# Kernel tuning notes

Hardware: AMD Instinct MI355X
Metric: run time of the kernel (lower is better)

The kernel has to match this reference:

```python
import jax, jax.numpy as jnp
import numpy as np
import math

B, L, D, H = 8, 1024, 768, 12
DH = D // H
MAX_NORM = 1.0 - 1e-5
EPS = 1e-15

def _beta_fn(a, b):
    return math.exp(math.lgamma(a) + math.lgamma(b) - math.lgamma(a + b))

# beta-split scaling factor from Hyperbolic Neural Networks++ (Shimizu et al.)
BETA_RATIO = _beta_fn(DH / 2.0, 0.5) / _beta_fn(D / 2.0, 0.5)

def _artanh(x):
    return jnp.arctanh(jnp.clip(x, -MAX_NORM, MAX_NORM))

def _norm(x):
    return jnp.sqrt(jnp.maximum(jnp.sum(x * x, -1, keepdims=True), EPS * EPS))

def _project(x):
    # clip points back inside the Poincare ball (c=1)
    return x * jnp.minimum(1.0, MAX_NORM / _norm(x))

def _expmap0(v):
    n = _norm(v)
    return jnp.tanh(n) * v / n

def _logmap0(x):
    n = _norm(x)
    return _artanh(n) * x / n

def _mobius_add(x, y):
    x2 = jnp.sum(x * x, -1, keepdims=True)
    y2 = jnp.sum(y * y, -1, keepdims=True)
    xy = jnp.sum(x * y, -1, keepdims=True)
    num = (1.0 + 2.0 * xy + y2) * x + (1.0 - x2) * y
    den = 1.0 + 2.0 * xy + x2 * y2
    return num / jnp.maximum(den, EPS)

def _mobius_matvec(W, x):
    xn = _norm(x)
    mx = x @ W.T
    mxn = _norm(mx)
    return _project(jnp.tanh(mxn / xn * _artanh(xn)) * mx / mxn)

def _hyp_linear(x, W, b=None):
    y = _mobius_matvec(W, x)
    if b is not None:
        y = _project(_mobius_add(y, b))
    return y

def _beta_split(x):
    # (..., D) -> (..., H, DH): logmap0, split heads, beta-rescale, expmap0
    v = _logmap0(x)
    v = v.reshape(v.shape[:-1] + (H, DH)) * BETA_RATIO
    return _expmap0(v)

def _beta_concat(x):
    # (..., H, DH) -> (..., D)
    v = _logmap0(x) / BETA_RATIO
    v = v.reshape(v.shape[:-2] + (D,))
    return _expmap0(v)

def _pairwise_dist(q, k):
    # closed form: d(x,y) = 2 artanh(||-x (+) y||),
    # ||-x (+) y||^2 = ||x-y||^2 / (1 - 2<x,y> + ||x||^2 ||y||^2)
    q2 = jnp.sum(q * q, -1)  # (B,H,Lq)
    k2 = jnp.sum(k * k, -1)  # (B,H,Lk)
    qk = jnp.einsum('bhqd,bhkd->bhqk', q, k)
    diff2 = jnp.maximum(q2[..., :, None] + k2[..., None, :] - 2.0 * qk, 0.0)
    den = jnp.maximum(1.0 - 2.0 * qk + q2[..., :, None] * k2[..., None, :], EPS)
    t = jnp.sqrt(jnp.maximum(diff2 / den, 0.0))
    return 2.0 * _artanh(t)

def _mobius_scalar_mul(r, x):
    n = _norm(x)
    return jnp.tanh(r * _artanh(n)) * x / n

def _weighted_midpoint(v, w):
    # v: (B,H,Lk,DH) points on ball, w: (B,H,Lq,Lk) weights (geoopt-style)
    lam = 2.0 / jnp.maximum(1.0 - jnp.sum(v * v, -1), EPS)  # conformal factor (B,H,Lk)
    den = jnp.einsum('bhqk,bhk->bhq', w, lam - 1.0)[..., None]
    den = jnp.where(jnp.abs(den) < 1e-10, 1e-10, den)
    nom = jnp.einsum('bhqk,bhkd->bhqd', w, lam[..., None] * v)
    two_mean = nom / den
    return _project(_mobius_scalar_mul(0.5, two_mean))


def setup_inputs() -> dict:
    key = jax.random.key(0)
    ks = jax.random.split(key, 7)
    # points inside the ball: expmap0 of small tangent vectors (norm ~0.55)
    x = _project(_expmap0(0.02 * jax.random.normal(ks[0], (B, L, D), jnp.float32)))
    Wq = jax.random.normal(ks[1], (D, D), jnp.float32) / math.sqrt(D)
    Wk = jax.random.normal(ks[2], (D, D), jnp.float32) / math.sqrt(D)
    Wv = jax.random.normal(ks[3], (D, D), jnp.float32) / math.sqrt(D)
    Wp = jax.random.normal(ks[4], (D, D), jnp.float32) / math.sqrt(D)
    bp = _project(0.01 * jax.random.normal(ks[5], (D,), jnp.float32))
    scale = jnp.array(1.0, jnp.float32)
    return {"x": x, "Wq": Wq, "Wk": Wk, "Wv": Wv, "Wp": Wp, "bp": bp, "scale": scale}


def reference(x, Wq, Wk, Wv, Wp, bp, scale):
    # q/k/v hyperbolic linear (no bias), beta-split into heads -> (B,H,L,DH)
    q = jnp.swapaxes(_beta_split(_hyp_linear(x, Wq)), 1, 2)
    k = jnp.swapaxes(_beta_split(_hyp_linear(x, Wk)), 1, 2)
    v = jnp.swapaxes(_beta_split(_hyp_linear(x, Wv)), 1, 2)
    attn = jax.nn.softmax(scale * -_pairwise_dist(q, k), axis=-1)  # (B,H,L,L)
    y = _weighted_midpoint(v, attn)                 # (B,H,L,DH)
    y = _beta_concat(jnp.swapaxes(y, 1, 2))         # (B,L,D)
    y = _hyp_linear(y, Wp, bp)
    return y, attn
```

## Files before the change

kernel.cpp:

```cpp
#include <hip/hip_runtime.h>
#include <hip/hip_bf16.h>
#include <math.h>

namespace {

constexpr int Bb = 8, Ll = 1024, Dd = 768, Hh = 12, DHh = 64;
constexpr int DDm = Dd * Dd;
constexpr float MAXN = 1.0f - 1e-5f;
constexpr float EPSf = 1e-15f;

typedef __attribute__((ext_vector_type(8))) short short8;
typedef __attribute__((ext_vector_type(4))) short short4v;
typedef __attribute__((ext_vector_type(4))) float f32x4;

__device__ __forceinline__ float wred64(float v) {
#pragma unroll
  for (int m = 32; m >= 1; m >>= 1) v += __shfl_xor(v, m, 64);
  return v;
}

__device__ __forceinline__ float artanh_(float x) {
  return 0.5f * logf((1.0f + x) / (1.0f - x));
}

__device__ __forceinline__ void bsplit(float x, unsigned short& h,
                                       unsigned short& l) {
  __hip_bfloat16 hb = __float2bfloat16(x);
  const float hf = __bfloat162float(hb);
  __hip_bfloat16 lb = __float2bfloat16(x - hf);
  h = *(unsigned short*)&hb;
  l = *(unsigned short*)&lb;
}

__device__ __forceinline__ unsigned short bhi(float x) {
  __hip_bfloat16 hb = __float2bfloat16(x);
  return *(unsigned short*)&hb;
}

__device__ __forceinline__ float bf2f(unsigned short u) {
  union { unsigned int i; float f; } cv;
  cv.i = ((unsigned int)u) << 16;
  return cv.f;
}

__device__ __forceinline__ void gll16(const unsigned short* g,
                                      unsigned short* l) {
  __builtin_amdgcn_global_load_lds(
      (const __attribute__((address_space(1))) void*)g,
      (__attribute__((address_space(3))) void*)l, 16, 0, 0);
}

__global__ __launch_bounds__(768) void k_cvtx(const float* __restrict__ x,
                                              unsigned short* __restrict__ hi,
                                              float* __restrict__ xn2a) {
  const int t = threadIdx.x;
  const int row = blockIdx.x;
  const int w = t >> 6, lane = t & 63;
  __shared__ float red[12];
  const float xe = x[(size_t)row * Dd + t];
  hi[(size_t)row * Dd + t] = bhi(xe);
  const float s = wred64(xe * xe);
  if (lane == 0) red[w] = s;
  __syncthreads();
  if (t == 0) {
    float tot = 0.0f;
#pragma unroll
    for (int i = 0; i < 12; i++) tot += red[i];
    xn2a[row] = tot;
  }
}

__global__ __launch_bounds__(256) void k_cvt4(
    const float* __restrict__ w0, const float* __restrict__ w1,
    const float* __restrict__ w2, const float* __restrict__ w3,
    unsigned short* __restrict__ hi) {
  const int z = blockIdx.z;
  const float* in = (z == 0) ? w0 : (z == 1) ? w1 : (z == 2) ? w2 : w3;
  const int i = blockIdx.x * 256 + threadIdx.x;
  if (i >= DDm / 4) return;
  float4 v = ((const float4*)in)[i];
  ((ushort4*)(hi + (size_t)z * DDm))[i] =
      make_ushort4(bhi(v.x), bhi(v.y), bhi(v.z), bhi(v.w));
}

__global__ __launch_bounds__(256) void k_gemm_bf16h(
    const unsigned short* __restrict__ Ahi,
    const unsigned short* __restrict__ Whi, float* __restrict__ C) {
  constexpr int K = Dd, N = Dd;
  const int z = blockIdx.z;
  const unsigned short* Bh = Whi + (size_t)z * DDm;
  float* Cz = C + (size_t)z * 8192 * N;
  __shared__ __align__(16) unsigned short sAh[128 * 32];
  __shared__ __align__(16) unsigned short sBh[128 * 32];
  const int t = threadIdx.x;
  const int l = t & 63, wid = t >> 6;
  const int wr = wid >> 1, wc = wid & 1;
  const int m0 = blockIdx.y * 128, n0 = blockIdx.x * 128;

  const int r0 = t >> 2;
  const int kfs = ((t & 3) ^ ((r0 >> 1) & 3)) << 3;
  const size_t ga0 = (size_t)(m0 + r0) * K + kfs;
  const size_t ga1 = (size_t)(m0 + r0 + 64) * K + kfs;
  const size_t gb0 = (size_t)(n0 + r0) * K + kfs;
  const size_t gb1 = (size_t)(n0 + r0 + 64) * K + kfs;
  unsigned short* dA0 = &sAh[t * 8];
  unsigned short* dA1 = &sAh[(t + 256) * 8];
  unsigned short* dB0 = &sBh[t * 8];
  unsigned short* dB1 = &sBh[(t + 256) * 8];

  const int lar = l & 15, lkf = l >> 4;

  f32x4 acc[4][4] = {};

  for (int k0 = 0; k0 < K; k0 += 32) {
    __syncthreads();
    gll16(&Ahi[ga0 + k0], dA0);
    gll16(&Ahi[ga1 + k0], dA1);
    gll16(&Bh[gb0 + k0], dB0);
    gll16(&Bh[gb1 + k0], dB1);
    __syncthreads();

    short8 ah[4], bh[4];
#pragma unroll
    for (int f = 0; f < 4; f++) {
      const int ra = wr * 64 + f * 16 + lar;
      const int ia = ra * 32 + ((lkf ^ ((ra >> 1) & 3)) << 3);
      ah[f] = *(const short8*)&sAh[ia];
      const int rb = wc * 64 + f * 16 + lar;
      const int ib = rb * 32 + ((lkf ^ ((rb >> 1) & 3)) << 3);
      bh[f] = *(const short8*)&sBh[ib];
    }
#pragma unroll
    for (int i = 0; i < 4; i++)
#pragma unroll
      for (int j = 0; j < 4; j++)
        acc[i][j] = __builtin_amdgcn_mfma_f32_16x16x32_bf16(ah[i], bh[j],
                                                            acc[i][j], 0, 0, 0);
  }

#pragma unroll
  for (int i = 0; i < 4; i++)
#pragma unroll
    for (int j = 0; j < 4; j++) {
      const int row = m0 + wr * 64 + i * 16 + (l >> 4) * 4;
      const int col = n0 + wc * 64 + j * 16 + (l & 15);
      const f32x4 v = acc[i][j];
#pragma unroll
      for (int q = 0; q < 4; q++) Cz[(size_t)(row + q) * N + col] = v[q];
    }
}

__global__ __launch_bounds__(768) void k_qkvt3(
    const float* __restrict__ xn2a,
    const float* __restrict__ mq, const float* __restrict__ mk,
    const float* __restrict__ mv,
    unsigned short* __restrict__ qhh, unsigned short* __restrict__ qhl,
    unsigned short* __restrict__ khh, unsigned short* __restrict__ khl,
    unsigned short* __restrict__ vhh, unsigned short* __restrict__ vhl_,
    float* __restrict__ q2n, float* __restrict__ k2n,
    float* __restrict__ lam1, float beta_ratio) {
  const int t = threadIdx.x;
  const int row = blockIdx.x;
  const int mi = blockIdx.y;
  const int b = row >> 10, l = row & 1023;
  const int w = t >> 6, lane = t & 63;
  __shared__ float red[12];

  const float* m = (mi == 0) ? mq : (mi == 1) ? mk : mv;
  const float me = m[(size_t)row * Dd + t];
  const float s2 = wred64(me * me);
  if (lane == 0) red[w] = s2;
  __syncthreads();
  float mn2 = 0.0f;
#pragma unroll
  for (int i = 0; i < 12; i++) mn2 += red[i];

  const float xn = sqrtf(fmaxf(xn2a[row], EPSf * EPSf));
  const float arx = artanh_(fminf(xn, MAXN));

  const float mxn = sqrtf(fmaxf(mn2, EPSf * EPSf));
  const float pn = tanhf(mxn / xn * arx);
  const float c1 = pn / mxn * fminf(1.0f, MAXN / fmaxf(pn, EPSf));
  const float nn = fmaxf(fminf(pn, MAXN), EPSf);
  const float c2 = artanh_(nn) / nn;
  const float ve = c2 * c1 * me * beta_ratio;
  const float hs = wred64(ve * ve);
  const float hn = sqrtf(fmaxf(hs, EPSf * EPSf));
  const float th = tanhf(hn);
  const float oe = th / hn * ve;
  const size_t hidx = (size_t)(b * Hh + w) * Ll + l;
  const size_t oidx = hidx * DHh + lane;
  unsigned short hu, lu;
  if (mi == 0) {
    bsplit(oe, hu, lu);
    qhh[oidx] = hu; qhl[oidx] = lu;
    if (lane == 0) q2n[hidx] = th * th;
  } else if (mi == 1) {
    bsplit(oe, hu, lu);
    khh[oidx] = hu; khl[oidx] = lu;
    if (lane == 0) k2n[hidx] = th * th;
  } else {
    const float lam = 2.0f / fmaxf(1.0f - th * th, EPSf);
    bsplit(lam * oe, hu, lu);
    vhh[oidx] = hu; vhl_[oidx] = lu;
    if (lane == 0) lam1[hidx] = lam - 1.0f;
  }
}

__global__ __launch_bounds__(256) void k_vt(const unsigned short* __restrict__ vh,
                                            const unsigned short* __restrict__ vl,
                                            unsigned short* __restrict__ th,
                                            unsigned short* __restrict__ tl) {
  __shared__ __align__(16) unsigned short sh[64 * 72];
  __shared__ __align__(16) unsigned short sl[64 * 72];
  const int t = threadIdx.x;
  const int bh = blockIdx.y, c = blockIdx.x;
  const size_t ibase = ((size_t)bh * Ll + c * 64) * DHh;
#pragma unroll
  for (int u = 0; u < 2; u++) {
    const int ch = t + u * 256, r = ch >> 3, f = ch & 7;
    *(short8*)&sh[r * 72 + f * 8] = *(const short8*)&vh[ibase + r * DHh + f * 8];
    *(short8*)&sl[r * 72 + f * 8] = *(const short8*)&vl[ibase + r * DHh + f * 8];
  }
  __syncthreads();
#pragma unroll
  for (int u = 0; u < 2; u++) {
    const int ch = t + u * 256, d = ch >> 3, kb = ch & 7;
    short8 oh, ol;
#pragma unroll
    for (int i = 0; i < 8; i++) {
      oh[i] = (short)sh[(kb * 8 + i) * 72 + d];
      ol[i] = (short)sl[(kb * 8 + i) * 72 + d];
    }
    const size_t ob = ((size_t)bh * DHh + d) * Ll + c * 64 + kb * 8;
    *(short8*)&th[ob] = oh;
    *(short8*)&tl[ob] = ol;
  }
}

__global__ __launch_bounds__(256) void k_attn1(
    const unsigned short* __restrict__ qhh, const unsigned short* __restrict__ qhl,
    const unsigned short* __restrict__ khh, const unsigned short* __restrict__ khl,
    const unsigned short* __restrict__ vth, const unsigned short* __restrict__ vtl,
    const float* __restrict__ q2n, const float* __restrict__ k2n,
    const float* __restrict__ lam1, const float* __restrict__ scale_p,
    float* __restrict__ attn, float* __restrict__ rowsum,
    float* __restrict__ yh) {
  __shared__ __align__(16) unsigned short kldsh[32 * 72];
  __shared__ __align__(16) unsigned short kldsl[32 * 72];
  __shared__ __align__(16) unsigned short vldsh[64 * 36];
  __shared__ __align__(16) unsigned short vldsl[64 * 36];
  __shared__ __align__(16) unsigned short wlds[4][16 * 36];
  __shared__ __align__(16) float k2s[32];
  __shared__ __align__(16) float l1s[32];
  __shared__ __align__(16) float ik2s[32];
  __shared__ float dred[4][16];
  const int t = threadIdx.x, l = t & 63, w = t >> 6;
  const int lr = l & 15, lg = l >> 4;
  const int bh = blockIdx.y, q0 = blockIdx.x * 64;
  const size_t hbase = (size_t)bh * Ll;
  const float scale = scale_p[0];
  const bool sone = (scale == 1.0f);

  short8 aqh[2], aql[2];
#pragma unroll
  for (int s = 0; s < 2; s++) {
    const size_t off = (hbase + q0 + w * 16 + lr) * (size_t)DHh + s * 32 + lg * 8;
    aqh[s] = *(const short8*)&qhh[off];
    aql[s] = *(const short8*)&qhl[off];
  }
  const float q2v = q2n[hbase + q0 + w * 16 + lr];

  const int kr = t >> 3, kf = t & 7;
  const int vd = t >> 2, vf = t & 3;

  float rs = 0.0f, dacc = 0.0f;
  f32x4 pv[4] = {};

  short8 pkh, pkl, pvh, pvl;
  float k2r = 0.0f, l1r = 0.0f;
  auto load_chunk = [&](int c) {
    const size_t kg = (hbase + c * 32 + kr) * (size_t)DHh + kf * 8;
    pkh = *(const short8*)&khh[kg];
    pkl = *(const short8*)&khl[kg];
    const size_t vg = ((size_t)bh * DHh + vd) * (size_t)Ll + c * 32 + vf * 8;
    pvh = *(const short8*)&vth[vg];
    pvl = *(const short8*)&vtl[vg];
    if (t < 32) {
      k2r = k2n[hbase + c * 32 + t];
      l1r = lam1[hbase + c * 32 + t];
    }
  };
  load_chunk(0);

  for (int c = 0; c < 32; c++) {
    __syncthreads();
    *(short8*)&kldsh[kr * 72 + kf * 8] = pkh;
    *(short8*)&kldsl[kr * 72 + kf * 8] = pkl;
    *(short8*)&vldsh[vd * 36 + vf * 8] = pvh;
    *(short8*)&vldsl[vd * 36 + vf * 8] = pvl;
    if (t < 32) {
      k2s[t] = k2r;
      l1s[t] = l1r;
      ik2s[t] = __builtin_amdgcn_rcpf(1.0f - k2r);
    }
    __syncthreads();
    if (c + 1 < 32) load_chunk(c + 1);

#pragma unroll
    for (int j = 0; j < 2; j++) {
      f32x4 acc = {};
#pragma unroll
      for (int s = 0; s < 2; s++) {
        const int ko = (j * 16 + lr) * 72 + s * 32 + lg * 8;
        const short8 kfh = *(const short8*)&kldsh[ko];
        const short8 kfl = *(const short8*)&kldsl[ko];
        acc = __builtin_amdgcn_mfma_f32_16x16x32_bf16(kfh, aqh[s], acc, 0, 0, 0);
        acc = __builtin_amdgcn_mfma_f32_16x16x32_bf16(kfh, aql[s], acc, 0, 0, 0);
        acc = __builtin_amdgcn_mfma_f32_16x16x32_bf16(kfl, aqh[s], acc, 0, 0, 0);
      }
      const float4 k2q = *(const float4*)&k2s[j * 16 + lg * 4];
      const float4 l1q = *(const float4*)&l1s[j * 16 + lg * 4];
      const float4 ikq = *(const float4*)&ik2s[j * 16 + lg * 4];
      const float kq[4] = {k2q.x, k2q.y, k2q.z, k2q.w};
      const float lq[4] = {l1q.x, l1q.y, l1q.z, l1q.w};
      const float iq[4] = {ikq.x, ikq.y, ikq.z, ikq.w};
      short4v wv;
#pragma unroll
      for (int r = 0; r < 4; r++) {
        const float qk2 = acc[r] + acc[r];
        const float d = fmaxf(q2v + kq[r] - qk2, 0.0f);
        const float dn = fmaf(q2v, kq[r], 1.0f) - qk2;
        const float m_ = fmaxf(d * dn, 1e-30f);
        const float s_ = m_ * __builtin_amdgcn_rsqf(m_);
        float e = (dn + d - s_ - s_) * iq[r];
        if (!sone) e = expf(scale * logf(fmaxf(e, 1e-30f)));
        rs += e;
        __hip_bfloat16 eb = __float2bfloat16(e);
        wv[r] = *(short*)&eb;
        dacc += __bfloat162float(eb) * lq[r];
      }
      *(short4v*)&wlds[w][lr * 36 + j * 16 + lg * 4] = wv;
    }
    {
      const short8 wa = *(const short8*)&wlds[w][lr * 36 + lg * 8];
#pragma unroll
      for (int n = 0; n < 4; n++) {
        const int bo = (n * 16 + lr) * 36 + lg * 8;
        const short8 vbh8 = *(const short8*)&vldsh[bo];
        const short8 vbl8 = *(const short8*)&vldsl[bo];
        pv[n] = __builtin_amdgcn_mfma_f32_16x16x32_bf16(wa, vbh8, pv[n], 0, 0, 0);
        pv[n] = __builtin_amdgcn_mfma_f32_16x16x32_bf16(wa, vbl8, pv[n], 0, 0, 0);
      }
    }
    {
      const int qy = l >> 2, cg = l & 3;
      const short8 ev = *(const short8*)&wlds[w][qy * 36 + cg * 8];
      unsigned short* eb =
          (unsigned short*)(attn + (hbase + q0 + w * 16 + qy) * (size_t)Ll);
      *(short8*)&eb[c * 32 + cg * 8] = ev;
    }
  }

  rs += __shfl_xor(rs, 16, 64);
  rs += __shfl_xor(rs, 32, 64);
  if (lg == 0) rowsum[hbase + q0 + w * 16 + lr] = rs;

  dacc += __shfl_xor(dacc, 16, 64);
  dacc += __shfl_xor(dacc, 32, 64);
  if (lg == 0) dred[w][lr] = dacc;

  const int b = bh / Hh, h = bh % Hh;
#pragma unroll
  for (int r = 0; r < 4; r++) {
    float den = dred[w][lg * 4 + r];
    if (fabsf(den) < 1e-10f) den = 1e-10f;
    const float dinv = 1.0f / den;
    float tm[4];
    float n2 = 0.0f;
#pragma unroll
    for (int n = 0; n < 4; n++) {
      tm[n] = pv[n][r] * dinv;
      n2 += tm[n] * tm[n];
    }
    n2 += __shfl_xor(n2, 1, 64);
    n2 += __shfl_xor(n2, 2, 64);
    n2 += __shfl_xor(n2, 4, 64);
    n2 += __shfl_xor(n2, 8, 64);
    const float nn = sqrtf(fmaxf(n2, EPSf * EPSf));
    const float nc = fminf(nn, MAXN);
    const float pn = nc / (1.0f + sqrtf(fmaxf(1.0f - nc * nc, 0.0f)));
    const float f = pn / nn * fminf(1.0f, MAXN / fmaxf(pn, EPSf));
    const int ql = q0 + w * 16 + lg * 4 + r;
#pragma unroll
    for (int n = 0; n < 4; n++)
      yh[(((size_t)(b * Ll + ql)) * Hh + h) * DHh + n * 16 + lr] = f * tm[n];
  }
}

__global__ __launch_bounds__(256) void k_norm(float* __restrict__ attn,
                                              const float* __restrict__ rowsum) {
  const int row = blockIdx.x;
  const float rinv = 1.0f / rowsum[row];
  float* prow = attn + (size_t)row * Ll;
  const ushort4 u4 = ((const ushort4*)prow)[threadIdx.x];
  __syncthreads();
  float4 v;
  v.x = bf2f(u4.x) * rinv;
  v.y = bf2f(u4.y) * rinv;
  v.z = bf2f(u4.z) * rinv;
  v.w = bf2f(u4.w) * rinv;
  ((float4*)prow)[threadIdx.x] = v;
}

__global__ __launch_bounds__(768) void k_concat(
    const float* __restrict__ yh, float* __restrict__ yc,
    unsigned short* __restrict__ ychi, float beta_ratio) {
  const int t = threadIdx.x;
  const int row = blockIdx.x;
  const int w = t >> 6, lane = t & 63;
  __shared__ float red[12];
  const float ye = yh[(size_t)row * Dd + t];
  const float hs = wred64(ye * ye);
  const float hn = sqrtf(fmaxf(hs, EPSf * EPSf));
  const float cc = artanh_(fminf(hn, MAXN)) / hn / beta_ratio;
  const float ve = cc * ye;
  const float s = wred64(ve * ve);
  if (lane == 0) red[w] = s;
  __syncthreads();
  float n2 = 0.0f;
#pragma unroll
  for (int i = 0; i < 12; i++) n2 += red[i];
  const float n = sqrtf(fmaxf(n2, EPSf * EPSf));
  const float f = tanhf(n) / n;
  const float o = f * ve;
  yc[(size_t)row * Dd + t] = o;
  ychi[(size_t)row * Dd + t] = bhi(o);
}

__global__ __launch_bounds__(768) void k_final(
    const float* __restrict__ yc, const float* __restrict__ mp,
    const float* __restrict__ bp, float* __restrict__ out) {
  const int t = threadIdx.x;
  const int row = blockIdx.x;
  const int w = t >> 6, lane = t & 63;
  __shared__ float red[12];
  auto blockSum = [&](float v) -> float {
    __syncthreads();
    const float s = wred64(v);
    if (lane == 0) red[w] = s;
    __syncthreads();
    float tot = 0.0f;
#pragma unroll
    for (int i = 0; i < 12; i++) tot += red[i];
    return tot;
  };
  const float xe = yc[(size_t)row * Dd + t];
  const float me = mp[(size_t)row * Dd + t];
  const float be = bp[t];
  const float xn2 = blockSum(xe * xe);
  const float xn = sqrtf(fmaxf(xn2, EPSf * EPSf));
  const float arx = artanh_(fminf(xn, MAXN));
  const float mn2 = blockSum(me * me);
  const float mxn = sqrtf(fmaxf(mn2, EPSf * EPSf));
  const float pn = tanhf(mxn / xn * arx);
  const float c1 = pn / mxn * fminf(1.0f, MAXN / fmaxf(pn, EPSf));
  const float mme = c1 * me;
  const float x2 = blockSum(mme * mme);
  const float y2 = blockSum(be * be);
  const float xy = blockSum(mme * be);
  const float nume = (1.0f + 2.0f * xy + y2) * mme + (1.0f - x2) * be;
  const float den = fmaxf(1.0f + 2.0f * xy + x2 * y2, EPSf);
  const float re = nume / den;
  const float rn2 = blockSum(re * re);
  const float rn = sqrtf(fmaxf(rn2, EPSf * EPSf));
  const float f = fminf(1.0f, MAXN / rn);
  out[(size_t)row * Dd + t] = f * re;
}

}

extern "C" void kernel_launch(void* const* d_in, const int* in_sizes, int n_in,
                              void* d_out, int out_size, void* d_ws,
                              size_t ws_size, hipStream_t stream) {
  const float* x = (const float*)d_in[0];
  const float* Wq = (const float*)d_in[1];
  const float* Wk = (const float*)d_in[2];
  const float* Wv = (const float*)d_in[3];
  const float* Wp = (const float*)d_in[4];
  const float* bp = (const float*)d_in[5];
  const float* scale = (const float*)d_in[6];

  float* out = (float*)d_out;
  float* y_out = out;
  float* attn = out + (size_t)Bb * Ll * Dd;

  const size_t NH = (size_t)Bb * Hh * Ll;
  const size_t RD = (size_t)Bb * Ll * Dd;

  unsigned short* u = (unsigned short*)d_ws;
  unsigned short* qhh = u;
  unsigned short* qhl = u + RD;
  unsigned short* khh = u + 2 * RD;
  unsigned short* khl = u + 3 * RD;
  unsigned short* vth = u + 4 * RD;
  unsigned short* vtl = u + 5 * RD;
  unsigned short* vhh = u + 6 * RD;
  unsigned short* vhl_ = u + 7 * RD;
  unsigned short* whi = u + 8 * RD;
  float* fb = (float*)(whi + 4 * (size_t)DDm);
  float* q2n = fb;
  float* k2n = fb + NH;
  float* lam1 = fb + 2 * NH;
  float* rowsum = fb + 3 * NH;
  float* xn2a = fb + 4 * NH;
  float* yh = (float*)(u + 6 * RD);
  float* yc = (float*)u;
  unsigned short* ychi = u + 2 * RD;
  float* mp = (float*)(u + 4 * RD);

  float* mq = attn;
  float* mk = attn + RD;
  float* mv = attn + 2 * RD;
  unsigned short* xhi = (unsigned short*)(attn + 3 * RD);

  const double br =
      exp(lgamma(DHh / 2.0) + lgamma(0.5) - lgamma(DHh / 2.0 + 0.5) -
          (lgamma(Dd / 2.0) + lgamma(0.5) - lgamma(Dd / 2.0 + 0.5)));
  const float beta_ratio = (float)br;

  (void)in_sizes; (void)n_in; (void)out_size; (void)ws_size;

  k_cvtx<<<dim3(Bb * Ll), dim3(768), 0, stream>>>(x, xhi, xn2a);
  k_cvt4<<<dim3(DDm / 4 / 256, 1, 4), dim3(256), 0, stream>>>(Wq, Wk, Wv, Wp,
                                                              whi);

  k_gemm_bf16h<<<dim3(Dd / 128, (Bb * Ll) / 128, 3), dim3(256), 0, stream>>>(
      xhi, whi, mq);

  k_qkvt3<<<dim3(Bb * Ll, 3), dim3(768), 0, stream>>>(
      xn2a, mq, mk, mv, qhh, qhl, khh, khl, vhh, vhl_, q2n, k2n, lam1,
      beta_ratio);

  k_vt<<<dim3(16, Bb * Hh), dim3(256), 0, stream>>>(vhh, vhl_, vth, vtl);

  k_attn1<<<dim3(16, Bb * Hh), dim3(256), 0, stream>>>(
      qhh, qhl, khh, khl, vth, vtl, q2n, k2n, lam1, scale, attn, rowsum, yh);

  k_norm<<<dim3((int)NH), dim3(256), 0, stream>>>(attn, rowsum);

  k_concat<<<dim3(Bb * Ll), dim3(768), 0, stream>>>(yh, yc, ychi, beta_ratio);

  k_gemm_bf16h<<<dim3(Dd / 128, (Bb * Ll) / 128, 1), dim3(256), 0, stream>>>(
      ychi, whi + 3 * (size_t)DDm, mp);

  k_final<<<dim3(Bb * Ll), dim3(768), 0, stream>>>(yc, mp, bp, y_out);
}
```

Baseline: 624.9 us.

## Drop bf16 low part of V and double-buffer K/V tiles in attention

V is now stored only as a single bf16 value instead of a hi/lo split pair. This halves V writes, the transpose work and V loads, and removes half of the PV MFMAs. The attention loop also double-buffers its K/V/scalar LDS tiles, so one barrier per chunk replaces two and the next chunk's global loads are issued before the barrier. The cost is lower precision in the weighted midpoint accumulation and more LDS use.

Result: faster. 612.0 us (-2.1%).

```diff
diff --git a/kernel.cpp b/kernel.cpp
--- a/kernel.cpp
+++ b/kernel.cpp
@@ -156,7 +156,7 @@
     const float* __restrict__ mv,
     unsigned short* __restrict__ qhh, unsigned short* __restrict__ qhl,
     unsigned short* __restrict__ khh, unsigned short* __restrict__ khl,
-    unsigned short* __restrict__ vhh, unsigned short* __restrict__ vhl_,
+    unsigned short* __restrict__ vhh,
     float* __restrict__ q2n, float* __restrict__ k2n,
     float* __restrict__ lam1, float beta_ratio) {
   const int t = threadIdx.x;
@@ -201,18 +201,14 @@
     if (lane == 0) k2n[hidx] = th * th;
   } else {
     const float lam = 2.0f / fmaxf(1.0f - th * th, EPSf);
-    bsplit(lam * oe, hu, lu);
-    vhh[oidx] = hu; vhl_[oidx] = lu;
+    vhh[oidx] = bhi(lam * oe);
     if (lane == 0) lam1[hidx] = lam - 1.0f;
   }
 }
 
 __global__ __launch_bounds__(256) void k_vt(const unsigned short* __restrict__ vh,
-                                            const unsigned short* __restrict__ vl,
-                                            unsigned short* __restrict__ th,
-                                            unsigned short* __restrict__ tl) {
+                                            unsigned short* __restrict__ th) {
   __shared__ __align__(16) unsigned short sh[64 * 72];
-  __shared__ __align__(16) unsigned short sl[64 * 72];
   const int t = threadIdx.x;
   const int bh = blockIdx.y, c = blockIdx.x;
   const size_t ibase = ((size_t)bh * Ll + c * 64) * DHh;
@@ -220,40 +216,34 @@
   for (int u = 0; u < 2; u++) {
     const int ch = t + u * 256, r = ch >> 3, f = ch & 7;
     *(short8*)&sh[r * 72 + f * 8] = *(const short8*)&vh[ibase + r * DHh + f * 8];
-    *(short8*)&sl[r * 72 + f * 8] = *(const short8*)&vl[ibase + r * DHh + f * 8];
   }
   __syncthreads();
 #pragma unroll
   for (int u = 0; u < 2; u++) {
     const int ch = t + u * 256, d = ch >> 3, kb = ch & 7;
-    short8 oh, ol;
-#pragma unroll
-    for (int i = 0; i < 8; i++) {
-      oh[i] = (short)sh[(kb * 8 + i) * 72 + d];
-      ol[i] = (short)sl[(kb * 8 + i) * 72 + d];
-    }
+    short8 oh;
+#pragma unroll
+    for (int i = 0; i < 8; i++) oh[i] = (short)sh[(kb * 8 + i) * 72 + d];
     const size_t ob = ((size_t)bh * DHh + d) * Ll + c * 64 + kb * 8;
     *(short8*)&th[ob] = oh;
-    *(short8*)&tl[ob] = ol;
   }
 }
 
 __global__ __launch_bounds__(256) void k_attn1(
     const unsigned short* __restrict__ qhh, const unsigned short* __restrict__ qhl,
     const unsigned short* __restrict__ khh, const unsigned short* __restrict__ khl,
-    const unsigned short* __restrict__ vth, const unsigned short* __restrict__ vtl,
+    const unsigned short* __restrict__ vth,
     const float* __restrict__ q2n, const float* __restrict__ k2n,
     const float* __restrict__ lam1, const float* __restrict__ scale_p,
     float* __restrict__ attn, float* __restrict__ rowsum,
     float* __restrict__ yh) {
-  __shared__ __align__(16) unsigned short kldsh[32 * 72];
-  __shared__ __align__(16) unsigned short kldsl[32 * 72];
-  __shared__ __align__(16) unsigned short vldsh[64 * 36];
-  __shared__ __align__(16) unsigned short vldsl[64 * 36];
+  __shared__ __align__(16) unsigned short kldsh[2][32 * 72];
+  __shared__ __align__(16) unsigned short kldsl[2][32 * 72];
+  __shared__ __align__(16) unsigned short vldsh[2][64 * 36];
   __shared__ __align__(16) unsigned short wlds[4][16 * 36];
-  __shared__ __align__(16) float k2s[32];
-  __shared__ __align__(16) float l1s[32];
-  __shared__ __align__(16) float ik2s[32];
+  __shared__ __align__(16) float k2s[2][32];
+  __shared__ __align__(16) float l1s[2][32];
+  __shared__ __align__(16) float ik2s[2][32];
   __shared__ float dred[4][16];
   const int t = threadIdx.x, l = t & 63, w = t >> 6;
   const int lr = l & 15, lg = l >> 4;
@@ -277,7 +267,7 @@
   float rs = 0.0f, dacc = 0.0f;
   f32x4 pv[4] = {};
 
-  short8 pkh, pkl, pvh, pvl;
+  short8 pkh, pkl, pvh;
   float k2r = 0.0f, l1r = 0.0f;
   auto load_chunk = [&](int c) {
     const size_t kg = (hbase + c * 32 + kr) * (size_t)DHh + kf * 8;
@@ -285,7 +275,6 @@
     pkl = *(const short8*)&khl[kg];
     const size_t vg = ((size_t)bh * DHh + vd) * (size_t)Ll + c * 32 + vf * 8;
     pvh = *(const short8*)&vth[vg];
-    pvl = *(const short8*)&vtl[vg];
     if (t < 32) {
       k2r = k2n[hbase + c * 32 + t];
       l1r = lam1[hbase + c * 32 + t];
@@ -294,18 +283,17 @@
   load_chunk(0);
 
   for (int c = 0; c < 32; c++) {
+    const int pb = c & 1;
+    *(short8*)&kldsh[pb][kr * 72 + kf * 8] = pkh;
+    *(short8*)&kldsl[pb][kr * 72 + kf * 8] = pkl;
+    *(short8*)&vldsh[pb][vd * 36 + vf * 8] = pvh;
+    if (t < 32) {
+      k2s[pb][t] = k2r;
+      l1s[pb][t] = l1r;
+      ik2s[pb][t] = __builtin_amdgcn_rcpf(1.0f - k2r);
+    }
+    if (c + 1 < 32) load_chunk(c + 1);
     __syncthreads();
-    *(short8*)&kldsh[kr * 72 + kf * 8] = pkh;
-    *(short8*)&kldsl[kr * 72 + kf * 8] = pkl;
-    *(short8*)&vldsh[vd * 36 + vf * 8] = pvh;
-    *(short8*)&vldsl[vd * 36 + vf * 8] = pvl;
-    if (t < 32) {
-      k2s[t] = k2r;
-      l1s[t] = l1r;
-      ik2s[t] = __builtin_amdgcn_rcpf(1.0f - k2r);
-    }
-    __syncthreads();
-    if (c + 1 < 32) load_chunk(c + 1);
 
 #pragma unroll
     for (int j = 0; j < 2; j++) {
@@ -313,15 +301,15 @@
 #pragma unroll
       for (int s = 0; s < 2; s++) {
         const int ko = (j * 16 + lr) * 72 + s * 32 + lg * 8;
-        const short8 kfh = *(const short8*)&kldsh[ko];
-        const short8 kfl = *(const short8*)&kldsl[ko];
+        const short8 kfh = *(const short8*)&kldsh[pb][ko];
+        const short8 kfl = *(const short8*)&kldsl[pb][ko];
         acc = __builtin_amdgcn_mfma_f32_16x16x32_bf16(kfh, aqh[s], acc, 0, 0, 0);
         acc = __builtin_amdgcn_mfma_f32_16x16x32_bf16(kfh, aql[s], acc, 0, 0, 0);
         acc = __builtin_amdgcn_mfma_f32_16x16x32_bf16(kfl, aqh[s], acc, 0, 0, 0);
       }
-      const float4 k2q = *(const float4*)&k2s[j * 16 + lg * 4];
-      const float4 l1q = *(const float4*)&l1s[j * 16 + lg * 4];
-      const float4 ikq = *(const float4*)&ik2s[j * 16 + lg * 4];
+      const float4 k2q = *(const float4*)&k2s[pb][j * 16 + lg * 4];
+      const float4 l1q = *(const float4*)&l1s[pb][j * 16 + lg * 4];
+      const float4 ikq = *(const float4*)&ik2s[pb][j * 16 + lg * 4];
       const float kq[4] = {k2q.x, k2q.y, k2q.z, k2q.w};
       const float lq[4] = {l1q.x, l1q.y, l1q.z, l1q.w};
       const float iq[4] = {ikq.x, ikq.y, ikq.z, ikq.w};
@@ -346,11 +334,8 @@
       const short8 wa = *(const short8*)&wlds[w][lr * 36 + lg * 8];
 #pragma unroll
       for (int n = 0; n < 4; n++) {
-        const int bo = (n * 16 + lr) * 36 + lg * 8;
-        const short8 vbh8 = *(const short8*)&vldsh[bo];
-        const short8 vbl8 = *(const short8*)&vldsl[bo];
+        const short8 vbh8 = *(const short8*)&vldsh[pb][(n * 16 + lr) * 36 + lg * 8];
         pv[n] = __builtin_amdgcn_mfma_f32_16x16x32_bf16(wa, vbh8, pv[n], 0, 0, 0);
-        pv[n] = __builtin_amdgcn_mfma_f32_16x16x32_bf16(wa, vbl8, pv[n], 0, 0, 0);
       }
     }
     {
@@ -504,9 +489,7 @@
   unsigned short* khh = u + 2 * RD;
   unsigned short* khl = u + 3 * RD;
   unsigned short* vth = u + 4 * RD;
-  unsigned short* vtl = u + 5 * RD;
   unsigned short* vhh = u + 6 * RD;
-  unsigned short* vhl_ = u + 7 * RD;
   unsigned short* whi = u + 8 * RD;
   float* fb = (float*)(whi + 4 * (size_t)DDm);
   float* q2n = fb;
@@ -539,13 +522,12 @@
       xhi, whi, mq);
 
   k_qkvt3<<<dim3(Bb * Ll, 3), dim3(768), 0, stream>>>(
-      xn2a, mq, mk, mv, qhh, qhl, khh, khl, vhh, vhl_, q2n, k2n, lam1,
-      beta_ratio);
-
-  k_vt<<<dim3(16, Bb * Hh), dim3(256), 0, stream>>>(vhh, vhl_, vth, vtl);
+      xn2a, mq, mk, mv, qhh, qhl, khh, khl, vhh, q2n, k2n, lam1, beta_ratio);
+
+  k_vt<<<dim3(16, Bb * Hh), dim3(256), 0, stream>>>(vhh, vth);
 
   k_attn1<<<dim3(16, Bb * Hh), dim3(256), 0, stream>>>(
-      qhh, qhl, khh, khl, vth, vtl, q2n, k2n, lam1, scale, attn, rowsum, yh);
+      qhh, qhl, khh, khl, vth, q2n, k2n, lam1, scale, attn, rowsum, yh);
 
   k_norm<<<dim3((int)NH), dim3(256), 0, stream>>>(attn, rowsum);
 
```
